# Kernel optimization log

Measured on AMD Instinct MI355X. Metric: run time of the kernel, lower is better.

The kernel has to match this reference:

```python
import jax, jax.numpy as jnp
import numpy as np

N_NODES = 20000
N_EDGES = 640000
D_IN = 128
D_OUT = 128


def _weighted_mean_aggr(x, src, dst, ew, n):
    # mean over incoming edges of (edge_weight * x_src) -> [n, d]
    msg = x[src] * ew[:, None]                          # [E, d]
    s = jax.ops.segment_sum(msg, dst, num_segments=n)   # [n, d]
    cnt = jax.ops.segment_sum(jnp.ones_like(ew), dst, num_segments=n)
    return s / jnp.maximum(cnt, 1.0)[:, None]


def setup_inputs() -> dict:
    key = jax.random.key(0)
    ks = jax.random.split(key, 12)
    scale_x = 1.0 / np.sqrt(D_IN)
    scale_h = 1.0 / np.sqrt(D_OUT)
    return {
        "X": jax.random.normal(ks[0], (N_NODES, D_IN), jnp.float32),
        "edge_index": jax.random.randint(ks[1], (2, N_EDGES), 0, N_NODES),
        "edge_weight": jax.random.uniform(ks[2], (N_EDGES,), jnp.float32),
        "H": jax.random.normal(ks[3], (N_NODES, D_OUT), jnp.float32),
        "C": jax.random.normal(ks[4], (N_NODES, D_OUT), jnp.float32),
        # stacked gate weights, gate order: [i, f, c, o]
        "Wx_l": jax.random.normal(ks[5], (4, D_IN, D_OUT), jnp.float32) * scale_x,
        "Wx_r": jax.random.normal(ks[6], (4, D_IN, D_OUT), jnp.float32) * scale_x,
        "bx": jnp.zeros((4, D_OUT), jnp.float32),
        "Wh_l": jax.random.normal(ks[7], (4, D_OUT, D_OUT), jnp.float32) * scale_h,
        "Wh_r": jax.random.normal(ks[8], (4, D_OUT, D_OUT), jnp.float32) * scale_h,
        "bh": jnp.zeros((4, D_OUT), jnp.float32),
        # peephole weights, order [i, f, o]
        "wc": jax.random.normal(ks[9], (3, D_OUT), jnp.float32) * scale_h,
        "bg": jnp.zeros((4, D_OUT), jnp.float32),
    }


def reference(X, edge_index, edge_weight, H, C, Wx_l, Wx_r, bx, Wh_l, Wh_r, bh, wc, bg):
    n = X.shape[0]
    src, dst = edge_index[0], edge_index[1]

    # Shared weighted-mean aggregations (identical graph for all 8 convs)
    aggX = _weighted_mean_aggr(X, src, dst, edge_weight, n)   # [N, D_IN]
    aggH = _weighted_mean_aggr(H, src, dst, edge_weight, n)   # [N, D_OUT]

    # WeightedSAGEConv per gate: lin_l(aggr) + lin_r(x) + bias; stacked over 4 gates
    Gx = jnp.einsum('nd,gdo->gno', aggX, Wx_l) + jnp.einsum('nd,gdo->gno', X, Wx_r) + bx[:, None, :]
    Gh = jnp.einsum('nd,gdo->gno', aggH, Wh_l) + jnp.einsum('nd,gdo->gno', H, Wh_r) + bh[:, None, :]
    G = Gx + Gh                                               # [4, N, D_OUT], order i,f,c,o

    I = jax.nn.sigmoid(G[0] + wc[0] * C + bg[0])
    F = jax.nn.sigmoid(G[1] + wc[1] * C + bg[1])
    T = jnp.tanh(G[2] + bg[2])
    C_new = F * C + I * T
    O = jax.nn.sigmoid(G[3] + wc[2] * C_new + bg[3])
    H_new = O * jnp.tanh(C_new)
    return (H_new, C_new)
```

## Files before the change

kernel.cpp:

```cpp
#include <hip/hip_runtime.h>
#include <math.h>

#define NN 20000
#define NE 640000
#define D  128
#define NSLICE 2500
#define NTILES 625
#define SUBSEG 40
#define SEGSTRIDE 160
#define NCHUNK 640
#define CHUNK 1000

typedef __attribute__((ext_vector_type(8))) short short8;
typedef __attribute__((ext_vector_type(4))) float floatx4;

static __device__ __forceinline__ unsigned short f2bf(float f) {
    union { float f; unsigned int u; } v; v.f = f;
    unsigned int u = v.u;
    u += 0x7fff + ((u >> 16) & 1);
    return (unsigned short)(u >> 16);
}
static __device__ __forceinline__ unsigned int pack2bf(float a, float b) {
    return (unsigned int)f2bf(a) | ((unsigned int)f2bf(b) << 16);
}
static __device__ __forceinline__ float bf_lo(unsigned int u) {
    union { unsigned int i; float f; } v; v.i = u << 16; return v.f;
}
static __device__ __forceinline__ float bf_hi(unsigned int u) {
    union { unsigned int i; float f; } v; v.i = u & 0xffff0000u; return v.f;
}
static __device__ __forceinline__ float sigm(float x) { return 1.f / (1.f + __expf(-x)); }
static __device__ __forceinline__ float tanhx(float x) { return 1.f - 2.f / (__expf(2.f * x) + 1.f); }

static __device__ __forceinline__ void load_lds16(const void* g, void* l) {
    __builtin_amdgcn_global_load_lds(
        (const __attribute__((address_space(1))) unsigned int*)g,
        (__attribute__((address_space(3))) unsigned int*)l, 16, 0, 0);
}

__global__ void __launch_bounds__(256)
prep_fill_kernel(const int* __restrict__ src, const int* __restrict__ dst,
                 const float* __restrict__ ew, int* __restrict__ cnt4,
                 unsigned int* __restrict__ s_p,
                 const float4* __restrict__ X4, const float4* __restrict__ H4,
                 unsigned int* __restrict__ XH32,
                 const float* __restrict__ Wx_l, const float* __restrict__ Wx_r,
                 const float* __restrict__ Wh_l, const float* __restrict__ Wh_r,
                 const float* __restrict__ bx, const float* __restrict__ bh,
                 const float* __restrict__ bg,
                 unsigned short* __restrict__ Wsz, float* __restrict__ bias) {
    int tid = threadIdx.x, b = blockIdx.x;

    int chunk = b >> 3, s = b & 7;
    int lo = s * NSLICE, hi = lo + NSLICE;
    int4 d4, sr4; float4 w4;
    bool fill = (tid < 250);
    if (fill) {
        int e0 = chunk * CHUNK + tid * 4;
        d4  = *(const int4*)(dst + e0);
        sr4 = *(const int4*)(src + e0);
        w4  = *(const float4*)(ew + e0);
    }

    if (b < 2560) {
        int t = b * 256 + tid;
        if (t < NE) {
            float4 x = X4[t];
            float4 h = H4[t];
            int n = t >> 5, q = t & 31;
            unsigned int* row = XH32 + n * 128;
            row[2 * q]          = pack2bf(x.x, x.y);
            row[2 * q + 1]      = pack2bf(x.z, x.w);
            row[64 + 2 * q]     = pack2bf(h.x, h.y);
            row[64 + 2 * q + 1] = pack2bf(h.z, h.w);
        }
    } else if (b < 2816) {
        int t = (b - 2560) * 256 + tid;
        int row = t >> 5;
        int g = row >> 9, k = row & 511;
        int o = (t & 31) * 4;
        const float* Wb; int kk;
        if (k < 128)      { Wb = Wx_l; kk = k; }
        else if (k < 256) { Wb = Wx_r; kk = k - 128; }
        else if (k < 384) { Wb = Wh_l; kk = k - 256; }
        else              { Wb = Wh_r; kk = k - 384; }
        float4 w = *(const float4*)(Wb + g * 16384 + kk * 128 + o);
        int ci = k >> 5, jg = (k >> 3) & 3, off = k & 7;
        unsigned short* wp = Wsz + ci * 16384 + jg * 4096 + (g * 128 + o) * 8 + off;
        wp[0]  = f2bf(w.x);
        wp[8]  = f2bf(w.y);
        wp[16] = f2bf(w.z);
        wp[24] = f2bf(w.w);
        if (k == 0) {
            int j0 = g * 128 + o;
#pragma unroll
            for (int i = 0; i < 4; ++i)
                bias[j0 + i] = bx[j0 + i] + bh[j0 + i] + bg[j0 + i];
        }
    }

    if (fill) {
        int dv[4] = {d4.x, d4.y, d4.z, d4.w};
        int sv[4] = {sr4.x, sr4.y, sr4.z, sr4.w};
        float wv[4] = {w4.x, w4.y, w4.z, w4.w};
#pragma unroll
        for (int k = 0; k < 4; ++k) {
            int d = dv[k];
            if (d >= lo && d < hi) {
                int q = (int)((unsigned)sv[k] / 5000u);
                int p = atomicAdd(&cnt4[d * 4 + q], 1);
                if (p < SUBSEG)
                    s_p[d * SEGSTRIDE + q * SUBSEG + p] =
                        (unsigned int)sv[k] | ((unsigned int)f2bf(wv[k]) << 16);
            }
        }
    }
}

__global__ void __launch_bounds__(256)
aggregate_kernel(const uint2* __restrict__ XH64,
                 const int* __restrict__ cnt4,
                 const unsigned int* __restrict__ s_p,
                 uint2* __restrict__ AGG64) {
    int wv = threadIdx.x >> 6, lane = threadIdx.x & 63;
    int b = blockIdx.x;
    int s = b & 7, j = b >> 3;
    int n = __builtin_amdgcn_readfirstlane(s * NSLICE + j * 4 + wv);
    int c0 = cnt4[n * 4 + 0];
    int c1 = cnt4[n * 4 + 1];
    int c2 = cnt4[n * 4 + 2];
    int c3 = cnt4[n * 4 + 3];
    int deg = c0 + c1 + c2 + c3;
    const unsigned int* segbase = s_p + (size_t)n * SEGSTRIDE;
    float a0 = 0.f, a1 = 0.f, a2 = 0.f, a3 = 0.f;

#pragma unroll
    for (int p = 0; p < 4; ++p) {
        int c = (p == 0) ? c0 : (p == 1) ? c1 : (p == 2) ? c2 : c3;
        int m = (c < SUBSEG) ? c : SUBSEG;
        const unsigned int* seg = segbase + p * SUBSEG;
        int i = 0;
        for (; i + 8 <= m; i += 8) {
            unsigned int e[8];
            uint2 u[8];
#pragma unroll
            for (int k = 0; k < 8; ++k) e[k] = seg[i + k];
#pragma unroll
            for (int k = 0; k < 8; ++k)
                u[k] = XH64[(size_t)(e[k] & 0xffff) * 64 + lane];
#pragma unroll
            for (int k = 0; k < 8; ++k) {
                float w = __int_as_float(e[k] & 0xffff0000u);
                a0 += bf_lo(u[k].x) * w;
                a1 += bf_hi(u[k].x) * w;
                a2 += bf_lo(u[k].y) * w;
                a3 += bf_hi(u[k].y) * w;
            }
        }
        for (; i + 4 <= m; i += 4) {
            unsigned int e[4];
            uint2 u[4];
#pragma unroll
            for (int k = 0; k < 4; ++k) e[k] = seg[i + k];
#pragma unroll
            for (int k = 0; k < 4; ++k)
                u[k] = XH64[(size_t)(e[k] & 0xffff) * 64 + lane];
#pragma unroll
            for (int k = 0; k < 4; ++k) {
                float w = __int_as_float(e[k] & 0xffff0000u);
                a0 += bf_lo(u[k].x) * w;
                a1 += bf_hi(u[k].x) * w;
                a2 += bf_lo(u[k].y) * w;
                a3 += bf_hi(u[k].y) * w;
            }
        }
        for (; i < m; ++i) {
            unsigned int e = seg[i];
            float w = __int_as_float(e & 0xffff0000u);
            uint2 u = XH64[(size_t)(e & 0xffff) * 64 + lane];
            a0 += bf_lo(u.x) * w;
            a1 += bf_hi(u.x) * w;
            a2 += bf_lo(u.y) * w;
            a3 += bf_hi(u.y) * w;
        }
    }

    float inv = (deg > 0) ? 1.0f / (float)deg : 1.0f;
    uint2 r;
    r.x = pack2bf(a0 * inv, a1 * inv);
    r.y = pack2bf(a2 * inv, a3 * inv);
    AGG64[(size_t)n * 64 + lane] = r;
}

__global__ void __launch_bounds__(256)
gemm_lstm_kernel(const unsigned short* __restrict__ XH,
                 const unsigned short* __restrict__ AGG,
                 const unsigned short* __restrict__ Wsz,
                 const float* __restrict__ bias,
                 const float* __restrict__ wc,
                 const float* __restrict__ C,
                 float* __restrict__ out) {
    __shared__ __align__(16) short Bs[2][8192];

    int tid = threadIdx.x;
    int wv = tid >> 6, lane = tid & 63;
    int lm = lane & 15, lq = lane >> 4;
    int bid = blockIdx.x;
    int m0 = (bid >> 1) * 32;
    int hb = (bid & 1) * 512;

    floatx4 acc[2][4];
#pragma unroll
    for (int mt = 0; mt < 2; ++mt)
#pragma unroll
        for (int g = 0; g < 4; ++g) acc[mt][g] = (floatx4)(0.f);

#pragma unroll
    for (int g = 0; g < 4; ++g)
        load_lds16(Wsz + wv * 4096 + g * 1024 + hb + lane * 8,
                   &Bs[0][wv * 2048 + g * 512]);

    short8 ca0, ca1;
    {
        const unsigned short* ar = AGG + (size_t)(m0 + lm) * 256 + lq * 8;
        ca0 = *(const short8*)ar;
        ca1 = *(const short8*)(ar + 16 * 256);
    }

    for (int it = 0; it < 16; ++it) {
        __syncthreads();
        if (it < 15) {
            const unsigned short* wb = Wsz + (it + 1) * 16384 + wv * 4096 + hb;
            short* lb = &Bs[(it + 1) & 1][wv * 2048];
#pragma unroll
            for (int g = 0; g < 4; ++g)
                load_lds16(wb + g * 1024 + lane * 8, &lb[g * 512]);
        }
        short8 na0, na1;
        if (it < 15) {
            int kn = (it + 1) * 32;
            const unsigned short* ab = (kn & 128) ? XH : AGG;
            int aoff = (kn & 127) | ((kn & 256) >> 1);
            const unsigned short* arn = ab + (size_t)(m0 + lm) * 256 + aoff + lq * 8;
            na0 = *(const short8*)arn;
            na1 = *(const short8*)(arn + 16 * 256);
        }
        const short* bsc = Bs[it & 1];
#pragma unroll
        for (int g = 0; g < 4; ++g) {
            short8 bfr = *(const short8*)&bsc[(lq << 11) + (g << 9) + ((wv << 4) + lm) * 8];
            acc[0][g] = __builtin_amdgcn_mfma_f32_16x16x32_bf16(ca0, bfr, acc[0][g], 0, 0, 0);
            acc[1][g] = __builtin_amdgcn_mfma_f32_16x16x32_bf16(ca1, bfr, acc[1][g], 0, 0, 0);
        }
        ca0 = na0; ca1 = na1;
    }

    int cg0 = (hb >> 3) + (wv << 4) + lm;
    float bG[4], wP[3];
#pragma unroll
    for (int g = 0; g < 4; ++g) bG[g] = bias[(g << 7) + cg0];
#pragma unroll
    for (int j = 0; j < 3; ++j) wP[j] = wc[j * 128 + cg0];

#pragma unroll
    for (int mt = 0; mt < 2; ++mt)
#pragma unroll
        for (int r = 0; r < 4; ++r) {
            int row = m0 + mt * 16 + lq * 4 + r;
            float c = C[(size_t)row * D + cg0];
            float pi = acc[mt][0][r] + bG[0] + wP[0] * c;
            float pf = acc[mt][1][r] + bG[1] + wP[1] * c;
            float pt = acc[mt][2][r] + bG[2];
            float po = acc[mt][3][r] + bG[3];
            float I = sigm(pi);
            float F = sigm(pf);
            float T = tanhx(pt);
            float cn = F * c + I * T;
            float O = sigm(po + wP[2] * cn);
            out[(size_t)row * D + cg0] = O * tanhx(cn);
            out[(size_t)NN * D + (size_t)row * D + cg0] = cn;
        }
}

extern "C" void kernel_launch(void* const* d_in, const int* in_sizes, int n_in,
                              void* d_out, int out_size, void* d_ws, size_t ws_size,
                              hipStream_t stream) {
    const float* X  = (const float*)d_in[0];
    const int* ei   = (const int*)d_in[1];
    const float* ew = (const float*)d_in[2];
    const float* H  = (const float*)d_in[3];
    const float* C  = (const float*)d_in[4];
    const float* Wx_l = (const float*)d_in[5];
    const float* Wx_r = (const float*)d_in[6];
    const float* bx   = (const float*)d_in[7];
    const float* Wh_l = (const float*)d_in[8];
    const float* Wh_r = (const float*)d_in[9];
    const float* bh   = (const float*)d_in[10];
    const float* wc   = (const float*)d_in[11];
    const float* bg   = (const float*)d_in[12];
    float* out = (float*)d_out;

    const int* src = ei;
    const int* dst = ei + NE;

    char* ws = (char*)d_ws;
    int* cnt4 = (int*)(ws + 0);
    unsigned int* s_p = (unsigned int*)(ws + 320128);
    unsigned short* XH  = (unsigned short*)(ws + 13120128);
    unsigned short* AGG = (unsigned short*)(ws + 23360128);
    unsigned short* Wsz = (unsigned short*)(ws + 33600128);
    float* bias = (float*)(ws + 34124416);

    hipMemsetAsync(cnt4, 0, NN * 4 * sizeof(int), stream);
    prep_fill_kernel<<<5120, 256, 0, stream>>>(src, dst, ew, cnt4, s_p,
                                               (const float4*)X, (const float4*)H,
                                               (unsigned int*)XH,
                                               Wx_l, Wx_r, Wh_l, Wh_r,
                                               bx, bh, bg, Wsz, bias);
    aggregate_kernel<<<NN / 4, 256, 0, stream>>>((const uint2*)XH, cnt4, s_p,
                                                 (uint2*)AGG);
    gemm_lstm_kernel<<<NTILES * 2, 256, 0, stream>>>(XH, AGG, Wsz, bias, wc, C, out);
}
```

Before: 200.6 us.

## Fuse neighbor aggregation into GEMM-LSTM kernel via swizzled LDS tile

Merges the separate aggregation kernel into the GEMM+LSTM kernel. Each block first gathers and averages neighbor features for its 32 rows into a swizzled LDS buffer, with 8 threads per row each handling 32 features. It then runs the MFMA GEMM over all 512 output columns, streaming weights directly from global memory into registers instead of staging them through LDS. This removes the AGG round trip through global memory and one kernel launch. In exchange it halves the grid to 625 blocks, changes the gather so each thread reads 64-byte chunks instead of wave-wide coalesced rows, and raises register pressure.

```diff
diff --git a/kernel.cpp b/kernel.cpp
--- a/kernel.cpp
+++ b/kernel.cpp
@@ -32,10 +32,11 @@
 static __device__ __forceinline__ float sigm(float x) { return 1.f / (1.f + __expf(-x)); }
 static __device__ __forceinline__ float tanhx(float x) { return 1.f - 2.f / (__expf(2.f * x) + 1.f); }
 
-static __device__ __forceinline__ void load_lds16(const void* g, void* l) {
-    __builtin_amdgcn_global_load_lds(
-        (const __attribute__((address_space(1))) unsigned int*)g,
-        (__attribute__((address_space(3))) unsigned int*)l, 16, 0, 0);
+static __device__ __forceinline__ void acc8(float* a, uint4 v, float wgt) {
+    a[0] += bf_lo(v.x) * wgt; a[1] += bf_hi(v.x) * wgt;
+    a[2] += bf_lo(v.y) * wgt; a[3] += bf_hi(v.y) * wgt;
+    a[4] += bf_lo(v.z) * wgt; a[5] += bf_hi(v.z) * wgt;
+    a[6] += bf_lo(v.w) * wgt; a[7] += bf_hi(v.w) * wgt;
 }
 
 __global__ void __launch_bounds__(256)
@@ -118,167 +119,189 @@
 }
 
 __global__ void __launch_bounds__(256)
-aggregate_kernel(const uint2* __restrict__ XH64,
-                 const int* __restrict__ cnt4,
-                 const unsigned int* __restrict__ s_p,
-                 uint2* __restrict__ AGG64) {
-    int wv = threadIdx.x >> 6, lane = threadIdx.x & 63;
-    int b = blockIdx.x;
-    int s = b & 7, j = b >> 3;
-    int n = __builtin_amdgcn_readfirstlane(s * NSLICE + j * 4 + wv);
-    int c0 = cnt4[n * 4 + 0];
-    int c1 = cnt4[n * 4 + 1];
-    int c2 = cnt4[n * 4 + 2];
-    int c3 = cnt4[n * 4 + 3];
-    int deg = c0 + c1 + c2 + c3;
-    const unsigned int* segbase = s_p + (size_t)n * SEGSTRIDE;
-    float a0 = 0.f, a1 = 0.f, a2 = 0.f, a3 = 0.f;
-
-#pragma unroll
-    for (int p = 0; p < 4; ++p) {
-        int c = (p == 0) ? c0 : (p == 1) ? c1 : (p == 2) ? c2 : c3;
-        int m = (c < SUBSEG) ? c : SUBSEG;
-        const unsigned int* seg = segbase + p * SUBSEG;
-        int i = 0;
-        for (; i + 8 <= m; i += 8) {
-            unsigned int e[8];
-            uint2 u[8];
-#pragma unroll
-            for (int k = 0; k < 8; ++k) e[k] = seg[i + k];
-#pragma unroll
-            for (int k = 0; k < 8; ++k)
-                u[k] = XH64[(size_t)(e[k] & 0xffff) * 64 + lane];
-#pragma unroll
-            for (int k = 0; k < 8; ++k) {
-                float w = __int_as_float(e[k] & 0xffff0000u);
-                a0 += bf_lo(u[k].x) * w;
-                a1 += bf_hi(u[k].x) * w;
-                a2 += bf_lo(u[k].y) * w;
-                a3 += bf_hi(u[k].y) * w;
-            }
-        }
-        for (; i + 4 <= m; i += 4) {
-            unsigned int e[4];
-            uint2 u[4];
-#pragma unroll
-            for (int k = 0; k < 4; ++k) e[k] = seg[i + k];
-#pragma unroll
-            for (int k = 0; k < 4; ++k)
-                u[k] = XH64[(size_t)(e[k] & 0xffff) * 64 + lane];
-#pragma unroll
-            for (int k = 0; k < 4; ++k) {
-                float w = __int_as_float(e[k] & 0xffff0000u);
-                a0 += bf_lo(u[k].x) * w;
-                a1 += bf_hi(u[k].x) * w;
-                a2 += bf_lo(u[k].y) * w;
-                a3 += bf_hi(u[k].y) * w;
-            }
-        }
-        for (; i < m; ++i) {
-            unsigned int e = seg[i];
-            float w = __int_as_float(e & 0xffff0000u);
-            uint2 u = XH64[(size_t)(e & 0xffff) * 64 + lane];
-            a0 += bf_lo(u.x) * w;
-            a1 += bf_hi(u.x) * w;
-            a2 += bf_lo(u.y) * w;
-            a3 += bf_hi(u.y) * w;
-        }
-    }
-
-    float inv = (deg > 0) ? 1.0f / (float)deg : 1.0f;
-    uint2 r;
-    r.x = pack2bf(a0 * inv, a1 * inv);
-    r.y = pack2bf(a2 * inv, a3 * inv);
-    AGG64[(size_t)n * 64 + lane] = r;
-}
-
-__global__ void __launch_bounds__(256)
-gemm_lstm_kernel(const unsigned short* __restrict__ XH,
-                 const unsigned short* __restrict__ AGG,
-                 const unsigned short* __restrict__ Wsz,
-                 const float* __restrict__ bias,
-                 const float* __restrict__ wc,
-                 const float* __restrict__ C,
-                 float* __restrict__ out) {
-    __shared__ __align__(16) short Bs[2][8192];
+aggemm_lstm_kernel(const unsigned short* __restrict__ XH,
+                   const int* __restrict__ cnt4,
+                   const unsigned int* __restrict__ s_p,
+                   const unsigned short* __restrict__ Wsz,
+                   const float* __restrict__ bias,
+                   const float* __restrict__ wc,
+                   const float* __restrict__ C,
+                   float* __restrict__ out) {
+    __shared__ __align__(16) char sA[16384];
 
     int tid = threadIdx.x;
     int wv = tid >> 6, lane = tid & 63;
     int lm = lane & 15, lq = lane >> 4;
-    int bid = blockIdx.x;
-    int m0 = (bid >> 1) * 32;
-    int hb = (bid & 1) * 512;
-
-    floatx4 acc[2][4];
+    int m0 = blockIdx.x * 32;
+
+    {
+        int rr = tid >> 3;
+        int cch = tid & 7;
+        int n = m0 + rr;
+        int4 cn = *(const int4*)(cnt4 + n * 4);
+        const unsigned int* segb = s_p + (size_t)n * SEGSTRIDE;
+        const uint4* xb = (const uint4*)XH + cch * 4;
+        float ac[32];
+#pragma unroll
+        for (int j = 0; j < 32; ++j) ac[j] = 0.f;
+        int deg = cn.x + cn.y + cn.z + cn.w;
+#pragma unroll
+        for (int q = 0; q < 4; ++q) {
+            int cq = (q == 0) ? cn.x : (q == 1) ? cn.y : (q == 2) ? cn.z : cn.w;
+            int mq = (cq < SUBSEG) ? cq : SUBSEG;
+            const unsigned int* seg = segb + q * SUBSEG;
+            int i = 0;
+            for (; i + 2 <= mq; i += 2) {
+                unsigned int e0 = seg[i], e1 = seg[i + 1];
+                const uint4* p0 = xb + (size_t)(e0 & 0xffff) * 32;
+                const uint4* p1 = xb + (size_t)(e1 & 0xffff) * 32;
+                uint4 v00 = p0[0], v01 = p0[1], v02 = p0[2], v03 = p0[3];
+                uint4 v10 = p1[0], v11 = p1[1], v12 = p1[2], v13 = p1[3];
+                float w0 = __int_as_float(e0 & 0xffff0000u);
+                float w1 = __int_as_float(e1 & 0xffff0000u);
+                acc8(ac +  0, v00, w0); acc8(ac +  8, v01, w0);
+                acc8(ac + 16, v02, w0); acc8(ac + 24, v03, w0);
+                acc8(ac +  0, v10, w1); acc8(ac +  8, v11, w1);
+                acc8(ac + 16, v12, w1); acc8(ac + 24, v13, w1);
+            }
+            if (i < mq) {
+                unsigned int e0 = seg[i];
+                const uint4* p0 = xb + (size_t)(e0 & 0xffff) * 32;
+                uint4 v00 = p0[0], v01 = p0[1], v02 = p0[2], v03 = p0[3];
+                float w0 = __int_as_float(e0 & 0xffff0000u);
+                acc8(ac +  0, v00, w0); acc8(ac +  8, v01, w0);
+                acc8(ac + 16, v02, w0); acc8(ac + 24, v03, w0);
+            }
+        }
+        float inv = (deg > 0) ? 1.0f / (float)deg : 1.0f;
+        int sw = (rr & 7) << 4;
+        int bb = rr * 512 + cch * 64;
+        uint4 o0, o1, o2, o3;
+        o0.x = pack2bf(ac[0] * inv, ac[1] * inv);   o0.y = pack2bf(ac[2] * inv, ac[3] * inv);
+        o0.z = pack2bf(ac[4] * inv, ac[5] * inv);   o0.w = pack2bf(ac[6] * inv, ac[7] * inv);
+        o1.x = pack2bf(ac[8] * inv, ac[9] * inv);   o1.y = pack2bf(ac[10] * inv, ac[11] * inv);
+        o1.z = pack2bf(ac[12] * inv, ac[13] * inv); o1.w = pack2bf(ac[14] * inv, ac[15] * inv);
+        o2.x = pack2bf(ac[16] * inv, ac[17] * inv); o2.y = pack2bf(ac[18] * inv, ac[19] * inv);
+        o2.z = pack2bf(ac[20] * inv, ac[21] * inv); o2.w = pack2bf(ac[22] * inv, ac[23] * inv);
+        o3.x = pack2bf(ac[24] * inv, ac[25] * inv); o3.y = pack2bf(ac[26] * inv, ac[27] * inv);
+        o3.z = pack2bf(ac[28] * inv, ac[29] * inv); o3.w = pack2bf(ac[30] * inv, ac[31] * inv);
+        *(uint4*)(sA + ((bb +  0) ^ sw)) = o0;
+        *(uint4*)(sA + ((bb + 16) ^ sw)) = o1;
+        *(uint4*)(sA + ((bb + 32) ^ sw)) = o2;
+        *(uint4*)(sA + ((bb + 48) ^ sw)) = o3;
+    }
+
+    floatx4 acc[2][4][2];
 #pragma unroll
     for (int mt = 0; mt < 2; ++mt)
 #pragma unroll
-        for (int g = 0; g < 4; ++g) acc[mt][g] = (floatx4)(0.f);
-
+        for (int g = 0; g < 4; ++g)
+#pragma unroll
+            for (int nt = 0; nt < 2; ++nt) acc[mt][g][nt] = (floatx4)(0.f);
+
+    const unsigned short* aBase = XH + (size_t)(m0 + lm) * 256 + lq * 8;
+    const unsigned short* wB = Wsz + lq * 4096 + (wv << 8) + lm * 8;
+
+    short8 ca0, ca1, cb[8];
+    ca0 = *(const short8*)(aBase);
+    ca1 = *(const short8*)(aBase + 16 * 256);
 #pragma unroll
     for (int g = 0; g < 4; ++g)
-        load_lds16(Wsz + wv * 4096 + g * 1024 + hb + lane * 8,
-                   &Bs[0][wv * 2048 + g * 512]);
-
-    short8 ca0, ca1;
-    {
-        const unsigned short* ar = AGG + (size_t)(m0 + lm) * 256 + lq * 8;
-        ca0 = *(const short8*)ar;
-        ca1 = *(const short8*)(ar + 16 * 256);
-    }
-
-    for (int it = 0; it < 16; ++it) {
-        __syncthreads();
-        if (it < 15) {
-            const unsigned short* wb = Wsz + (it + 1) * 16384 + wv * 4096 + hb;
-            short* lb = &Bs[(it + 1) & 1][wv * 2048];
+#pragma unroll
+        for (int nt = 0; nt < 2; ++nt)
+            cb[g * 2 + nt] = *(const short8*)(wB + 4 * 16384 + g * 1024 + nt * 128);
+
+    for (int it = 0; it < 8; ++it) {
+        short8 na0, na1, nb[8];
+        if (it < 7) {
+            const unsigned short* ar = aBase + (it + 1) * 32;
+            na0 = *(const short8*)(ar);
+            na1 = *(const short8*)(ar + 16 * 256);
+            int ci = it + 5 + ((it + 1) & 4);
+            const unsigned short* wb2 = wB + ci * 16384;
 #pragma unroll
             for (int g = 0; g < 4; ++g)
-                load_lds16(wb + g * 1024 + lane * 8, &lb[g * 512]);
-        }
-        short8 na0, na1;
-        if (it < 15) {
-            int kn = (it + 1) * 32;
-            const unsigned short* ab = (kn & 128) ? XH : AGG;
-            int aoff = (kn & 127) | ((kn & 256) >> 1);
-            const unsigned short* arn = ab + (size_t)(m0 + lm) * 256 + aoff + lq * 8;
-            na0 = *(const short8*)arn;
-            na1 = *(const short8*)(arn + 16 * 256);
-        }
-        const short* bsc = Bs[it & 1];
-#pragma unroll
-        for (int g = 0; g < 4; ++g) {
-            short8 bfr = *(const short8*)&bsc[(lq << 11) + (g << 9) + ((wv << 4) + lm) * 8];
-            acc[0][g] = __builtin_amdgcn_mfma_f32_16x16x32_bf16(ca0, bfr, acc[0][g], 0, 0, 0);
-            acc[1][g] = __builtin_amdgcn_mfma_f32_16x16x32_bf16(ca1, bfr, acc[1][g], 0, 0, 0);
-        }
+#pragma unroll
+                for (int nt = 0; nt < 2; ++nt)
+                    nb[g * 2 + nt] = *(const short8*)(wb2 + g * 1024 + nt * 128);
+        }
+#pragma unroll
+        for (int g = 0; g < 4; ++g)
+#pragma unroll
+            for (int nt = 0; nt < 2; ++nt) {
+                acc[0][g][nt] = __builtin_amdgcn_mfma_f32_16x16x32_bf16(ca0, cb[g * 2 + nt], acc[0][g][nt], 0, 0, 0);
+                acc[1][g][nt] = __builtin_amdgcn_mfma_f32_16x16x32_bf16(ca1, cb[g * 2 + nt], acc[1][g][nt], 0, 0, 0);
+            }
         ca0 = na0; ca1 = na1;
-    }
-
-    int cg0 = (hb >> 3) + (wv << 4) + lm;
-    float bG[4], wP[3];
-#pragma unroll
-    for (int g = 0; g < 4; ++g) bG[g] = bias[(g << 7) + cg0];
-#pragma unroll
-    for (int j = 0; j < 3; ++j) wP[j] = wc[j * 128 + cg0];
+#pragma unroll
+        for (int k = 0; k < 8; ++k) cb[k] = nb[k];
+    }
+
+#pragma unroll
+    for (int g = 0; g < 4; ++g)
+#pragma unroll
+        for (int nt = 0; nt < 2; ++nt)
+            cb[g * 2 + nt] = *(const short8*)(wB + g * 1024 + nt * 128);
+
+    __syncthreads();
+
+    int swr = (lm & 7) << 4;
+    for (int it = 0; it < 8; ++it) {
+        short8 nb[8];
+        if (it < 7) {
+            int ci = it + 1 + ((it + 1) & 4);
+            const unsigned short* wb2 = wB + ci * 16384;
+#pragma unroll
+            for (int g = 0; g < 4; ++g)
+#pragma unroll
+                for (int nt = 0; nt < 2; ++nt)
+                    nb[g * 2 + nt] = *(const short8*)(wb2 + g * 1024 + nt * 128);
+        }
+        int b0 = (lm * 512 + it * 64 + lq * 16) ^ swr;
+        short8 la0 = *(const short8*)(sA + b0);
+        short8 la1 = *(const short8*)(sA + b0 + 8192);
+#pragma unroll
+        for (int g = 0; g < 4; ++g)
+#pragma unroll
+            for (int nt = 0; nt < 2; ++nt) {
+                acc[0][g][nt] = __builtin_amdgcn_mfma_f32_16x16x32_bf16(la0, cb[g * 2 + nt], acc[0][g][nt], 0, 0, 0);
+                acc[1][g][nt] = __builtin_amdgcn_mfma_f32_16x16x32_bf16(la1, cb[g * 2 + nt], acc[1][g][nt], 0, 0, 0);
+            }
+#pragma unroll
+        for (int k = 0; k < 8; ++k) cb[k] = nb[k];
+    }
+
+    float bG[4][2], wP[3][2];
+#pragma unroll
+    for (int nt = 0; nt < 2; ++nt) {
+        int cg0 = (wv << 5) + (nt << 4) + lm;
+#pragma unroll
+        for (int g = 0; g < 4; ++g) bG[g][nt] = bias[(g << 7) + cg0];
+#pragma unroll
+        for (int j = 0; j < 3; ++j) wP[j][nt] = wc[j * 128 + cg0];
+    }
 
 #pragma unroll
     for (int mt = 0; mt < 2; ++mt)
 #pragma unroll
         for (int r = 0; r < 4; ++r) {
             int row = m0 + mt * 16 + lq * 4 + r;
-            float c = C[(size_t)row * D + cg0];
-            float pi = acc[mt][0][r] + bG[0] + wP[0] * c;
-            float pf = acc[mt][1][r] + bG[1] + wP[1] * c;
-            float pt = acc[mt][2][r] + bG[2];
-            float po = acc[mt][3][r] + bG[3];
-            float I = sigm(pi);
-            float F = sigm(pf);
-            float T = tanhx(pt);
-            float cn = F * c + I * T;
-            float O = sigm(po + wP[2] * cn);
-            out[(size_t)row * D + cg0] = O * tanhx(cn);
-            out[(size_t)NN * D + (size_t)row * D + cg0] = cn;
+#pragma unroll
+            for (int nt = 0; nt < 2; ++nt) {
+                int cg0 = (wv << 5) + (nt << 4) + lm;
+                float c = C[(size_t)row * D + cg0];
+                float pi = acc[mt][0][nt][r] + bG[0][nt] + wP[0][nt] * c;
+                float pf = acc[mt][1][nt][r] + bG[1][nt] + wP[1][nt] * c;
+                float pt = acc[mt][2][nt][r] + bG[2][nt];
+                float po = acc[mt][3][nt][r] + bG[3][nt];
+                float I = sigm(pi);
+                float F = sigm(pf);
+                float T = tanhx(pt);
+                float cn = F * c + I * T;
+                float O = sigm(po + wP[2][nt] * cn);
+                out[(size_t)row * D + cg0] = O * tanhx(cn);
+                out[(size_t)NN * D + (size_t)row * D + cg0] = cn;
+            }
         }
 }
 
@@ -307,9 +330,8 @@
     int* cnt4 = (int*)(ws + 0);
     unsigned int* s_p = (unsigned int*)(ws + 320128);
     unsigned short* XH  = (unsigned short*)(ws + 13120128);
-    unsigned short* AGG = (unsigned short*)(ws + 23360128);
-    unsigned short* Wsz = (unsigned short*)(ws + 33600128);
-    float* bias = (float*)(ws + 34124416);
+    unsigned short* Wsz = (unsigned short*)(ws + 23360128);
+    float* bias = (float*)(ws + 23884416);
 
     hipMemsetAsync(cnt4, 0, NN * 4 * sizeof(int), stream);
     prep_fill_kernel<<<5120, 256, 0, stream>>>(src, dst, ew, cnt4, s_p,
@@ -317,7 +339,6 @@
                                                (unsigned int*)XH,
                                                Wx_l, Wx_r, Wh_l, Wh_r,
                                                bx, bh, bg, Wsz, bias);
-    aggregate_kernel<<<NN / 4, 256, 0, stream>>>((const uint2*)XH, cnt4, s_p,
-                                                 (uint2*)AGG);
-    gemm_lstm_kernel<<<NTILES * 2, 256, 0, stream>>>(XH, AGG, Wsz, bias, wc, C, out);
-}
+    aggemm_lstm_kernel<<<NTILES, 256, 0, stream>>>(XH, cnt4, s_p, Wsz, bias,
+                                                   wc, C, out);
+}
```

New measurement: 211.1 us. 5.2% more time.

## Stage 64-row A tiles in swizzled LDS and stream weights through registers

Applied to the files above, without the earlier changes.

The fused GEMM+LSTM kernel now handles 64 rows per block instead of 32. It loads the full XH and AGG rows once into 64 KB of LDS, using an XOR swizzle to avoid bank conflicts. Weight fragments are read straight from global memory into registers with one-step prefetch, and the k-chunk order is remapped to match the LDS layout, which removes the per-iteration barrier. The grid shrinks to 626 blocks, and a row guard covers the partial last tile. In exchange, the large LDS footprint limits occupancy and the last tile reads past the valid rows.

```diff
diff --git a/kernel.cpp b/kernel.cpp
--- a/kernel.cpp
+++ b/kernel.cpp
@@ -5,10 +5,8 @@
 #define NE 640000
 #define D  128
 #define NSLICE 2500
-#define NTILES 625
 #define SUBSEG 40
 #define SEGSTRIDE 160
-#define NCHUNK 640
 #define CHUNK 1000
 
 typedef __attribute__((ext_vector_type(8))) short short8;
@@ -200,59 +198,70 @@
                  const float* __restrict__ wc,
                  const float* __restrict__ C,
                  float* __restrict__ out) {
-    __shared__ __align__(16) short Bs[2][8192];
+    __shared__ __align__(16) char sA[65536];
 
     int tid = threadIdx.x;
     int wv = tid >> 6, lane = tid & 63;
     int lm = lane & 15, lq = lane >> 4;
     int bid = blockIdx.x;
-    int m0 = (bid >> 1) * 32;
+    int m0 = (bid >> 1) * 64;
     int hb = (bid & 1) * 512;
 
-    floatx4 acc[2][4];
-#pragma unroll
-    for (int mt = 0; mt < 2; ++mt)
+    {
+        int lrow = (lane >> 5);
+        int gofs = ((lane & 31) * 16) ^ ((lrow & 7) << 4);
+#pragma unroll
+        for (int j = 0; j < 8; ++j) {
+            int r0 = wv * 16 + j * 2;
+            int rw = r0 + lrow;
+            int go = ((lane & 31) * 16) ^ ((rw & 7) << 4);
+            load_lds16(XH + (size_t)(m0 + rw) * 256 + (go >> 1),
+                       sA + r0 * 512);
+            load_lds16(AGG + (size_t)(m0 + rw) * 256 + (go >> 1),
+                       sA + 32768 + r0 * 512);
+        }
+        (void)gofs; (void)lrow;
+    }
+
+    floatx4 acc[4][4];
+#pragma unroll
+    for (int mt = 0; mt < 4; ++mt)
 #pragma unroll
         for (int g = 0; g < 4; ++g) acc[mt][g] = (floatx4)(0.f);
 
-#pragma unroll
-    for (int g = 0; g < 4; ++g)
-        load_lds16(Wsz + wv * 4096 + g * 1024 + hb + lane * 8,
-                   &Bs[0][wv * 2048 + g * 512]);
-
-    short8 ca0, ca1;
-    {
-        const unsigned short* ar = AGG + (size_t)(m0 + lm) * 256 + lq * 8;
-        ca0 = *(const short8*)ar;
-        ca1 = *(const short8*)(ar + 16 * 256);
-    }
-
+    const unsigned short* wB = Wsz + lq * 4096 + hb + ((wv << 4) + lm) * 8;
+
+    short8 cb0 = *(const short8*)(wB + 4 * 16384);
+    short8 cb1 = *(const short8*)(wB + 4 * 16384 + 1024);
+    short8 cb2 = *(const short8*)(wB + 4 * 16384 + 2048);
+    short8 cb3 = *(const short8*)(wB + 4 * 16384 + 3072);
+
+    __syncthreads();
+
+    int swr = (lm & 7) << 4;
     for (int it = 0; it < 16; ++it) {
-        __syncthreads();
+        short8 nb0, nb1, nb2, nb3;
         if (it < 15) {
-            const unsigned short* wb = Wsz + (it + 1) * 16384 + wv * 4096 + hb;
-            short* lb = &Bs[(it + 1) & 1][wv * 2048];
-#pragma unroll
-            for (int g = 0; g < 4; ++g)
-                load_lds16(wb + g * 1024 + lane * 8, &lb[g * 512]);
-        }
-        short8 na0, na1;
-        if (it < 15) {
-            int kn = (it + 1) * 32;
-            const unsigned short* ab = (kn & 128) ? XH : AGG;
-            int aoff = (kn & 127) | ((kn & 256) >> 1);
-            const unsigned short* arn = ab + (size_t)(m0 + lm) * 256 + aoff + lq * 8;
-            na0 = *(const short8*)arn;
-            na1 = *(const short8*)(arn + 16 * 256);
-        }
-        const short* bsc = Bs[it & 1];
-#pragma unroll
-        for (int g = 0; g < 4; ++g) {
-            short8 bfr = *(const short8*)&bsc[(lq << 11) + (g << 9) + ((wv << 4) + lm) * 8];
-            acc[0][g] = __builtin_amdgcn_mfma_f32_16x16x32_bf16(ca0, bfr, acc[0][g], 0, 0, 0);
-            acc[1][g] = __builtin_amdgcn_mfma_f32_16x16x32_bf16(ca1, bfr, acc[1][g], 0, 0, 0);
-        }
-        ca0 = na0; ca1 = na1;
+            int itn = it + 1;
+            int ci = (itn < 8) ? (itn + 4 + (itn & 4)) : ((itn - 8) + ((itn - 8) & 4));
+            const unsigned short* wb2 = wB + ci * 16384;
+            nb0 = *(const short8*)(wb2);
+            nb1 = *(const short8*)(wb2 + 1024);
+            nb2 = *(const short8*)(wb2 + 2048);
+            nb3 = *(const short8*)(wb2 + 3072);
+        }
+        int pbase = (it < 8) ? 0 : 32768;
+        int koff = (it & 7) * 64 + lq * 16;
+#pragma unroll
+        for (int mt = 0; mt < 4; ++mt) {
+            int b0 = pbase + (mt * 16 + lm) * 512 + (koff ^ swr);
+            short8 a = *(const short8*)(sA + b0);
+            acc[mt][0] = __builtin_amdgcn_mfma_f32_16x16x32_bf16(a, cb0, acc[mt][0], 0, 0, 0);
+            acc[mt][1] = __builtin_amdgcn_mfma_f32_16x16x32_bf16(a, cb1, acc[mt][1], 0, 0, 0);
+            acc[mt][2] = __builtin_amdgcn_mfma_f32_16x16x32_bf16(a, cb2, acc[mt][2], 0, 0, 0);
+            acc[mt][3] = __builtin_amdgcn_mfma_f32_16x16x32_bf16(a, cb3, acc[mt][3], 0, 0, 0);
+        }
+        cb0 = nb0; cb1 = nb1; cb2 = nb2; cb3 = nb3;
     }
 
     int cg0 = (hb >> 3) + (wv << 4) + lm;
@@ -263,22 +272,24 @@
     for (int j = 0; j < 3; ++j) wP[j] = wc[j * 128 + cg0];
 
 #pragma unroll
-    for (int mt = 0; mt < 2; ++mt)
+    for (int mt = 0; mt < 4; ++mt)
 #pragma unroll
         for (int r = 0; r < 4; ++r) {
             int row = m0 + mt * 16 + lq * 4 + r;
-            float c = C[(size_t)row * D + cg0];
-            float pi = acc[mt][0][r] + bG[0] + wP[0] * c;
-            float pf = acc[mt][1][r] + bG[1] + wP[1] * c;
-            float pt = acc[mt][2][r] + bG[2];
-            float po = acc[mt][3][r] + bG[3];
-            float I = sigm(pi);
-            float F = sigm(pf);
-            float T = tanhx(pt);
-            float cn = F * c + I * T;
-            float O = sigm(po + wP[2] * cn);
-            out[(size_t)row * D + cg0] = O * tanhx(cn);
-            out[(size_t)NN * D + (size_t)row * D + cg0] = cn;
+            if (row < NN) {
+                float c = C[(size_t)row * D + cg0];
+                float pi = acc[mt][0][r] + bG[0] + wP[0] * c;
+                float pf = acc[mt][1][r] + bG[1] + wP[1] * c;
+                float pt = acc[mt][2][r] + bG[2];
+                float po = acc[mt][3][r] + bG[3];
+                float I = sigm(pi);
+                float F = sigm(pf);
+                float T = tanhx(pt);
+                float cn = F * c + I * T;
+                float O = sigm(po + wP[2] * cn);
+                out[(size_t)row * D + cg0] = O * tanhx(cn);
+                out[(size_t)NN * D + (size_t)row * D + cg0] = cn;
+            }
         }
 }
 
@@ -319,5 +330,5 @@
                                                bx, bh, bg, Wsz, bias);
     aggregate_kernel<<<NN / 4, 256, 0, stream>>>((const uint2*)XH, cnt4, s_p,
                                                  (uint2*)AGG);
-    gemm_lstm_kernel<<<NTILES * 2, 256, 0, stream>>>(XH, AGG, Wsz, bias, wc, C, out);
-}
+    gemm_lstm_kernel<<<626, 256, 0, stream>>>(XH, AGG, Wsz, bias, wc, C, out);
+}
```

Result: no change. 197.4 us (-1.6%).
